# Kernel optimization log

Hardware: AMD Instinct MI355X
Metric: run time of the kernel (lower is better)

## Reference

```python
import jax, jax.numpy as jnp
import numpy as np

F8_MAX = 448.0  # max representable value of float8_e4m3fn


def setup_inputs() -> dict:
    key = jax.random.key(0)
    k1, k2, k3 = jax.random.split(key, 3)
    inp = jax.random.normal(k1, (4, 2048, 4096), dtype=jnp.float32)
    weight = jax.random.normal(k2, (4096, 16384), dtype=jnp.float32) * 0.02  # [in, out] (stored transposed)
    bias = jax.random.normal(k3, (16384,), dtype=jnp.float32)
    return {"inp": inp, "weight": weight, "bias": bias}


def reference(inp, weight, bias):
    # --- weight quantization (from_float with abs-max observer) ---
    w_scale = jnp.max(jnp.abs(weight)) / F8_MAX                      # scalar fp32
    w_q = (weight * (1.0 / w_scale)).astype(jnp.float8_e4m3fn)       # [in, out] fp8

    # --- dynamic input quantization: amax = max(|min|, |max|) ---
    x = inp.reshape(-1, inp.shape[-1])                               # [N, in]
    amax = jnp.maximum(jnp.abs(jnp.min(x)), jnp.abs(jnp.max(x)))
    x_scale = amax / F8_MAX
    x_q = (x * (1.0 / x_scale)).astype(jnp.float8_e4m3fn)            # [N, in] fp8

    # --- fp8_gemm_v2: dequant-matmul with fused scales + bias ---
    out = jnp.matmul(x_q.astype(jnp.float32), w_q.astype(jnp.float32))
    out = out * (x_scale * w_scale) + bias                           # [N, out]
    return out.reshape(inp.shape[:-1] + (weight.shape[1],))
```

## Files before the change

kernel.cpp:

```cpp
#include <hip/hip_runtime.h>
#include <stdint.h>
#include <stddef.h>

typedef float f32x16 __attribute__((ext_vector_type(16)));
typedef int i32x8 __attribute__((ext_vector_type(8)));

union Frag32 { long l[4]; i32x8 v; };


__global__ void absmax_kernel(const float4* __restrict__ x, size_t n4,
                              unsigned int* __restrict__ out) {
  size_t idx = ((size_t)blockIdx.x * blockDim.x + threadIdx.x) * 2;
  size_t stride = (size_t)gridDim.x * blockDim.x * 2;
  float m0 = 0.f, m1 = 0.f;
  for (size_t i = idx; i < n4; i += stride) {
    float4 v = x[i];
    float4 u = x[i + 1];
    m0 = fmaxf(m0, fmaxf(fmaxf(fabsf(v.x), fabsf(v.y)),
                         fmaxf(fabsf(v.z), fabsf(v.w))));
    m1 = fmaxf(m1, fmaxf(fmaxf(fabsf(u.x), fabsf(u.y)),
                         fmaxf(fabsf(u.z), fabsf(u.w))));
  }
  float m = fmaxf(m0, m1);
#pragma unroll
  for (int off = 32; off > 0; off >>= 1)
    m = fmaxf(m, __shfl_xor(m, off));
  if ((threadIdx.x & 63) == 0)
    atomicMax(out, __float_as_uint(m));
}

__global__ void quantize_x_kernel(const float4* __restrict__ x,
                                  uint8_t* __restrict__ xq,
                                  const unsigned int* __restrict__ amax,
                                  int K, int n_chunks) {
  const float x_scale = __uint_as_float(amax[1]) / 448.0f;
  const float inv = 1.0f / x_scale;
  const int kslots = K >> 5;
  int idx = blockIdx.x * blockDim.x + threadIdx.x;
  const int stride = gridDim.x * blockDim.x;
  for (; idx < n_chunks; idx += stride) {
    const int slot = idx >> 9;
    const int p16 = idx & 511;
    const int row = p16 >> 1;
    const int kkb0 = (p16 & 1) << 4;
    const int mblk = slot / kslots;
    const int ksl = slot - mblk * kslots;
    const size_t f4 = ((size_t)(mblk * 256 + row) * K + ksl * 32 + kkb0) >> 2;
    const float4 v0 = x[f4 + 0], v1 = x[f4 + 1], v2 = x[f4 + 2], v3 = x[f4 + 3];
    uint32_t c0 = __builtin_amdgcn_cvt_pk_fp8_f32(v0.x * inv, v0.y * inv, 0, false);
    c0 = __builtin_amdgcn_cvt_pk_fp8_f32(v0.z * inv, v0.w * inv, c0, true);
    uint32_t c1 = __builtin_amdgcn_cvt_pk_fp8_f32(v1.x * inv, v1.y * inv, 0, false);
    c1 = __builtin_amdgcn_cvt_pk_fp8_f32(v1.z * inv, v1.w * inv, c1, true);
    uint32_t c2 = __builtin_amdgcn_cvt_pk_fp8_f32(v2.x * inv, v2.y * inv, 0, false);
    c2 = __builtin_amdgcn_cvt_pk_fp8_f32(v2.z * inv, v2.w * inv, c2, true);
    uint32_t c3 = __builtin_amdgcn_cvt_pk_fp8_f32(v3.x * inv, v3.y * inv, 0, false);
    c3 = __builtin_amdgcn_cvt_pk_fp8_f32(v3.z * inv, v3.w * inv, c3, true);
    const int paddr = (row * 32 + kkb0) ^ (((row >> 2) & 1) << 4);
    uint4 o;
    o.x = c0; o.y = c1; o.z = c2; o.w = c3;
    *(uint4*)(xq + (size_t)slot * 8192 + paddr) = o;
  }
}

__global__ void quantize_wT_kernel(const float* __restrict__ w,
                                   uint8_t* __restrict__ wqt,
                                   const unsigned int* __restrict__ amax,
                                   int N, int K) {
  __shared__ float tileF[64][129];
  const float w_scale = __uint_as_float(amax[0]) / 448.0f;
  const float inv = 1.0f / w_scale;
  const int tn = blockIdx.x;
  const int tk = blockIdx.y;
  const int t = threadIdx.x;
  {
    const int nn4 = t & 15;
    const int kk0 = t >> 4;
#pragma unroll
    for (int i = 0; i < 8; ++i) {
      const int kk = kk0 + i * 16;
      const float4 v =
          *(const float4*)&w[(size_t)(tk * 128 + kk) * N + tn * 64 + nn4 * 4];
      tileF[nn4 * 4 + 0][kk] = v.x;
      tileF[nn4 * 4 + 1][kk] = v.y;
      tileF[nn4 * 4 + 2][kk] = v.z;
      tileF[nn4 * 4 + 3][kk] = v.w;
    }
  }
  __syncthreads();
  {
    const int n = t & 63;
    const int c = t >> 6;
    unsigned long long q[4];
#pragma unroll
    for (int cc = 0; cc < 4; ++cc) {
      const float4 u0 = *(const float4*)&tileF[n][c * 32 + cc * 8];
      const float4 u1 = *(const float4*)&tileF[n][c * 32 + cc * 8 + 4];
      uint32_t lo = __builtin_amdgcn_cvt_pk_fp8_f32(u0.x * inv, u0.y * inv, 0, false);
      lo = __builtin_amdgcn_cvt_pk_fp8_f32(u0.z * inv, u0.w * inv, lo, true);
      uint32_t hi = __builtin_amdgcn_cvt_pk_fp8_f32(u1.x * inv, u1.y * inv, 0, false);
      hi = __builtin_amdgcn_cvt_pk_fp8_f32(u1.z * inv, u1.w * inv, hi, true);
      q[cc] = (unsigned long long)lo | ((unsigned long long)hi << 32);
    }
    const int n_g = tn * 64 + n;
    const int k0g = tk * 128 + c * 32;
    const size_t slot = (size_t)(n_g >> 8) * (K >> 5) + (k0g >> 5);
    const int row = n_g & 255;
    const int bit = (row >> 2) & 1;
    uint8_t* pbase = wqt + slot * 8192 + row * 32;
    ulonglong2 s0, s1;
    s0.x = q[0]; s0.y = q[1];
    s1.x = q[2]; s1.y = q[3];
    *(ulonglong2*)(pbase + (bit << 4)) = s0;
    *(ulonglong2*)(pbase + ((bit ^ 1) << 4)) = s1;
  }
}

#define T_BM 256
#define T_BN 256
#define UNIT_SCALE 0x7F7F7F7F

__device__ __forceinline__ void gl_lds16(const uint8_t* g, uint8_t* lds) {
  __builtin_amdgcn_global_load_lds(
      (const __attribute__((address_space(1))) void*)g,
      (__attribute__((address_space(3))) void*)lds, 16, 0, 0);
}

__global__ __launch_bounds__(1024, 4) void gemm_fp8_mx(
    const uint8_t* __restrict__ Aq, const uint8_t* __restrict__ BqT,
    const float* __restrict__ bias, const unsigned int* __restrict__ amax,
    float* __restrict__ C, int M, int N, int K) {
  extern __shared__ uint8_t smem[];
  uint8_t* const Ar = smem;
  uint8_t* const Br = smem + 65536;

  const int ntn = N / T_BN;
  const int bid = blockIdx.x;
  const int m0 = (bid / ntn) * T_BM;
  const int n0 = (bid % ntn) * T_BN;

  const int tid = threadIdx.x;
  const int w = tid >> 6;
  const int l = tid & 63;
  const int wr = w >> 2;
  const int wc = w & 3;

  const int kslots = K >> 5;

  const int soff = w * 1024 + l * 16;
  const uint8_t* a_src = Aq + (size_t)(m0 >> 8) * kslots * 8192 + soff;
  const uint8_t* b_src = BqT + (size_t)(n0 >> 8) * kslots * 8192 + soff;

  const int h = l >> 5;
  const int rl = l & 31;
  int aoff[2][2], boff[2][2];
#pragma unroll
  for (int mt = 0; mt < 2; ++mt) {
    const int ra = wr * 64 + mt * 32 + rl;
    const int rb = wc * 64 + mt * 32 + rl;
#pragma unroll
    for (int c = 0; c < 2; ++c) {
      aoff[mt][c] = h * 8192 + ra * 32 + ((c ^ ((ra >> 2) & 1)) << 4);
      boff[mt][c] = h * 8192 + rb * 32 + ((c ^ ((rb >> 2) & 1)) << 4);
    }
  }

  f32x16 acc[2][2];
#pragma unroll
  for (int i = 0; i < 2; ++i)
#pragma unroll
    for (int j = 0; j < 2; ++j) acc[i][j] = 0.f;

  const int NP = K >> 6;

  gl_lds16(a_src, Ar + soff);
  gl_lds16(b_src, Br + soff);
  gl_lds16(a_src + 16384, Ar + 16384 + soff);
  gl_lds16(b_src + 16384, Br + 16384 + soff);
  asm volatile("s_waitcnt vmcnt(2)" ::: "memory");
  __builtin_amdgcn_s_barrier();

#define PHASE_(pp)                                                          \
  do {                                                                      \
    const int ss = ((pp) + 2 < NP) ? ((pp) + 2) : ((pp)-2);                 \
    const int rslot = (((pp) + 2) & 3) * 16384;                             \
    gl_lds16(a_src + (size_t)ss * 16384, Ar + rslot + soff);                \
    gl_lds16(b_src + (size_t)ss * 16384, Br + rslot + soff);                \
    const uint8_t* Asl = Ar + ((pp)&3) * 16384;                             \
    const uint8_t* Bsl = Br + ((pp)&3) * 16384;                             \
    Frag32 af[2], bf[2];                                                    \
    _Pragma("unroll") for (int mt = 0; mt < 2; ++mt) {                      \
      ulonglong2 ta0 = *(const ulonglong2*)(Asl + aoff[mt][0]);             \
      ulonglong2 ta1 = *(const ulonglong2*)(Asl + aoff[mt][1]);             \
      af[mt].l[0] = (long)ta0.x; af[mt].l[1] = (long)ta0.y;                 \
      af[mt].l[2] = (long)ta1.x; af[mt].l[3] = (long)ta1.y;                 \
      ulonglong2 tb0 = *(const ulonglong2*)(Bsl + boff[mt][0]);             \
      ulonglong2 tb1 = *(const ulonglong2*)(Bsl + boff[mt][1]);             \
      bf[mt].l[0] = (long)tb0.x; bf[mt].l[1] = (long)tb0.y;                 \
      bf[mt].l[2] = (long)tb1.x; bf[mt].l[3] = (long)tb1.y;                 \
    }                                                                       \
    __builtin_amdgcn_s_setprio(1);                                          \
    acc[0][0] = __builtin_amdgcn_mfma_scale_f32_32x32x64_f8f6f4(            \
        af[0].v, bf[0].v, acc[0][0], 0, 0, 0, UNIT_SCALE, 0, UNIT_SCALE);   \
    acc[1][0] = __builtin_amdgcn_mfma_scale_f32_32x32x64_f8f6f4(            \
        af[1].v, bf[0].v, acc[1][0], 0, 0, 0, UNIT_SCALE, 0, UNIT_SCALE);   \
    acc[0][1] = __builtin_amdgcn_mfma_scale_f32_32x32x64_f8f6f4(            \
        af[0].v, bf[1].v, acc[0][1], 0, 0, 0, UNIT_SCALE, 0, UNIT_SCALE);   \
    acc[1][1] = __builtin_amdgcn_mfma_scale_f32_32x32x64_f8f6f4(            \
        af[1].v, bf[1].v, acc[1][1], 0, 0, 0, UNIT_SCALE, 0, UNIT_SCALE);   \
    __builtin_amdgcn_s_setprio(0);                                          \
    asm volatile("s_waitcnt vmcnt(2)" ::: "memory");                        \
  } while (0)

  for (int p = 0; p < NP; p += 2) {
    PHASE_(p);
    PHASE_(p + 1);
    __builtin_amdgcn_s_barrier();
  }
  asm volatile("s_waitcnt vmcnt(0)" ::: "memory");

  const float x_scale = __uint_as_float(amax[1]) / 448.0f;
  const float w_scale = __uint_as_float(amax[0]) / 448.0f;
  const float s = x_scale * w_scale;
  const int colb = n0 + wc * 64 + rl;
  const int rowb = m0 + wr * 64 + 4 * h;
#pragma unroll
  for (int nt = 0; nt < 2; ++nt) {
    const int col = colb + nt * 32;
    const float bv = bias[col];
#pragma unroll
    for (int mt = 0; mt < 2; ++mt) {
#pragma unroll
      for (int r = 0; r < 16; ++r) {
        const int row = rowb + mt * 32 + (r & 3) + 8 * (r >> 2);
        C[(size_t)row * N + col] = acc[mt][nt][r] * s + bv;
      }
    }
  }
}

extern "C" void kernel_launch(void* const* d_in, const int* in_sizes, int n_in,
                              void* d_out, int out_size, void* d_ws, size_t ws_size,
                              hipStream_t stream) {
  const float* inp = (const float*)d_in[0];
  const float* weight = (const float*)d_in[1];
  const float* bias = (const float*)d_in[2];
  float* out = (float*)d_out;

  const int N = in_sizes[2];
  const int K = in_sizes[1] / N;
  const int M = in_sizes[0] / K;

  uint8_t* ws = (uint8_t*)d_ws;
  unsigned int* amax = (unsigned int*)ws;
  uint8_t* xq = ws + 256;
  uint8_t* wqt = ws + 256 + (size_t)M * K;

  hipMemsetAsync(d_ws, 0, 8, stream);

  absmax_kernel<<<2048, 256, 0, stream>>>((const float4*)weight,
                                          (size_t)K * N / 4, amax + 0);
  absmax_kernel<<<2048, 256, 0, stream>>>((const float4*)inp,
                                          (size_t)M * K / 4, amax + 1);

  quantize_x_kernel<<<4096, 256, 0, stream>>>((const float4*)inp, xq, amax,
                                              K, M * K / 16);
  quantize_wT_kernel<<<dim3(N / 64, K / 128), 256, 0, stream>>>(weight, wqt,
                                                                amax, N, K);

  gemm_fp8_mx<<<(M / T_BM) * (N / T_BN), 1024, 131072, stream>>>(
      xq, wqt, bias, amax, out, M, N, K);
}
```

Before: 904.9 us.

## Load B fragments straight from global, halve LDS, and remap workgroups across XCDs

The weight (B) operand tiles are no longer staged in LDS. Each wave reads its B fragments directly from global memory into registers, so shared memory drops to 64KB and holds only the A ring buffer. The pipeline becomes one phase per iteration with a barrier each step, and workgroup IDs are remapped so consecutive blocks on the same XCD share weight columns. The aim is to cut LDS traffic and footprint and to improve L2 locality. In exchange, each B fragment is fetched four times per workgroup from cache, and the global load latency is waited on in the same iteration that uses it.

```diff
diff --git a/kernel.cpp b/kernel.cpp
--- a/kernel.cpp
+++ b/kernel.cpp
@@ -131,12 +131,16 @@
     float* __restrict__ C, int M, int N, int K) {
   extern __shared__ uint8_t smem[];
   uint8_t* const Ar = smem;
-  uint8_t* const Br = smem + 65536;
-
-  const int ntn = N / T_BN;
+
+  const int nwg = gridDim.x;
+  const int cpx = nwg >> 3;
   const int bid = blockIdx.x;
-  const int m0 = (bid / ntn) * T_BM;
-  const int n0 = (bid % ntn) * T_BN;
+  const int wg = (bid & 7) * cpx + (bid >> 3);
+  const int ntm = M / T_BM;
+  const int tm = wg & (ntm - 1);
+  const int tn = wg / ntm;
+  const int m0 = tm * T_BM;
+  const int n0 = tn * T_BN;
 
   const int tid = threadIdx.x;
   const int w = tid >> 6;
@@ -148,7 +152,6 @@
 
   const int soff = w * 1024 + l * 16;
   const uint8_t* a_src = Aq + (size_t)(m0 >> 8) * kslots * 8192 + soff;
-  const uint8_t* b_src = BqT + (size_t)(n0 >> 8) * kslots * 8192 + soff;
 
   const int h = l >> 5;
   const int rl = l & 31;
@@ -163,6 +166,7 @@
       boff[mt][c] = h * 8192 + rb * 32 + ((c ^ ((rb >> 2) & 1)) << 4);
     }
   }
+  const uint8_t* b_blk = BqT + (size_t)(n0 >> 8) * kslots * 8192;
 
   f32x16 acc[2][2];
 #pragma unroll
@@ -173,47 +177,47 @@
   const int NP = K >> 6;
 
   gl_lds16(a_src, Ar + soff);
-  gl_lds16(b_src, Br + soff);
   gl_lds16(a_src + 16384, Ar + 16384 + soff);
-  gl_lds16(b_src + 16384, Br + 16384 + soff);
-  asm volatile("s_waitcnt vmcnt(2)" ::: "memory");
+  asm volatile("s_waitcnt vmcnt(1)" ::: "memory");
   __builtin_amdgcn_s_barrier();
 
-#define PHASE_(pp)                                                          \
-  do {                                                                      \
-    const int ss = ((pp) + 2 < NP) ? ((pp) + 2) : ((pp)-2);                 \
-    const int rslot = (((pp) + 2) & 3) * 16384;                             \
-    gl_lds16(a_src + (size_t)ss * 16384, Ar + rslot + soff);                \
-    gl_lds16(b_src + (size_t)ss * 16384, Br + rslot + soff);                \
-    const uint8_t* Asl = Ar + ((pp)&3) * 16384;                             \
-    const uint8_t* Bsl = Br + ((pp)&3) * 16384;                             \
-    Frag32 af[2], bf[2];                                                    \
-    _Pragma("unroll") for (int mt = 0; mt < 2; ++mt) {                      \
-      ulonglong2 ta0 = *(const ulonglong2*)(Asl + aoff[mt][0]);             \
-      ulonglong2 ta1 = *(const ulonglong2*)(Asl + aoff[mt][1]);             \
-      af[mt].l[0] = (long)ta0.x; af[mt].l[1] = (long)ta0.y;                 \
-      af[mt].l[2] = (long)ta1.x; af[mt].l[3] = (long)ta1.y;                 \
-      ulonglong2 tb0 = *(const ulonglong2*)(Bsl + boff[mt][0]);             \
-      ulonglong2 tb1 = *(const ulonglong2*)(Bsl + boff[mt][1]);             \
-      bf[mt].l[0] = (long)tb0.x; bf[mt].l[1] = (long)tb0.y;                 \
-      bf[mt].l[2] = (long)tb1.x; bf[mt].l[3] = (long)tb1.y;                 \
-    }                                                                       \
-    __builtin_amdgcn_s_setprio(1);                                          \
-    acc[0][0] = __builtin_amdgcn_mfma_scale_f32_32x32x64_f8f6f4(            \
-        af[0].v, bf[0].v, acc[0][0], 0, 0, 0, UNIT_SCALE, 0, UNIT_SCALE);   \
-    acc[1][0] = __builtin_amdgcn_mfma_scale_f32_32x32x64_f8f6f4(            \
-        af[1].v, bf[0].v, acc[1][0], 0, 0, 0, UNIT_SCALE, 0, UNIT_SCALE);   \
-    acc[0][1] = __builtin_amdgcn_mfma_scale_f32_32x32x64_f8f6f4(            \
-        af[0].v, bf[1].v, acc[0][1], 0, 0, 0, UNIT_SCALE, 0, UNIT_SCALE);   \
-    acc[1][1] = __builtin_amdgcn_mfma_scale_f32_32x32x64_f8f6f4(            \
-        af[1].v, bf[1].v, acc[1][1], 0, 0, 0, UNIT_SCALE, 0, UNIT_SCALE);   \
-    __builtin_amdgcn_s_setprio(0);                                          \
-    asm volatile("s_waitcnt vmcnt(2)" ::: "memory");                        \
-  } while (0)
-
-  for (int p = 0; p < NP; p += 2) {
-    PHASE_(p);
-    PHASE_(p + 1);
+  for (int p = 0; p < NP; ++p) {
+    const uint8_t* bp = b_blk + (size_t)p * 16384;
+    Frag32 bf[2];
+#pragma unroll
+    for (int mt = 0; mt < 2; ++mt) {
+      ulonglong2 t0 = *(const ulonglong2*)(bp + boff[mt][0]);
+      ulonglong2 t1 = *(const ulonglong2*)(bp + boff[mt][1]);
+      bf[mt].l[0] = (long)t0.x; bf[mt].l[1] = (long)t0.y;
+      bf[mt].l[2] = (long)t1.x; bf[mt].l[3] = (long)t1.y;
+    }
+
+    const int ss = (p + 2 < NP) ? (p + 2) : (NP - 1);
+    gl_lds16(a_src + (size_t)ss * 16384, Ar + ((p + 2) & 3) * 16384 + soff);
+
+    const uint8_t* Asl = Ar + (p & 3) * 16384;
+    Frag32 af[2];
+#pragma unroll
+    for (int mt = 0; mt < 2; ++mt) {
+      ulonglong2 t0 = *(const ulonglong2*)(Asl + aoff[mt][0]);
+      ulonglong2 t1 = *(const ulonglong2*)(Asl + aoff[mt][1]);
+      af[mt].l[0] = (long)t0.x; af[mt].l[1] = (long)t0.y;
+      af[mt].l[2] = (long)t1.x; af[mt].l[3] = (long)t1.y;
+    }
+
+    asm volatile("s_waitcnt vmcnt(1)" ::: "memory");
+
+    __builtin_amdgcn_s_setprio(1);
+    acc[0][0] = __builtin_amdgcn_mfma_scale_f32_32x32x64_f8f6f4(
+        af[0].v, bf[0].v, acc[0][0], 0, 0, 0, UNIT_SCALE, 0, UNIT_SCALE);
+    acc[1][0] = __builtin_amdgcn_mfma_scale_f32_32x32x64_f8f6f4(
+        af[1].v, bf[0].v, acc[1][0], 0, 0, 0, UNIT_SCALE, 0, UNIT_SCALE);
+    acc[0][1] = __builtin_amdgcn_mfma_scale_f32_32x32x64_f8f6f4(
+        af[0].v, bf[1].v, acc[0][1], 0, 0, 0, UNIT_SCALE, 0, UNIT_SCALE);
+    acc[1][1] = __builtin_amdgcn_mfma_scale_f32_32x32x64_f8f6f4(
+        af[1].v, bf[1].v, acc[1][1], 0, 0, 0, UNIT_SCALE, 0, UNIT_SCALE);
+    __builtin_amdgcn_s_setprio(0);
+
     __builtin_amdgcn_s_barrier();
   }
   asm volatile("s_waitcnt vmcnt(0)" ::: "memory");
@@ -267,6 +271,6 @@
   quantize_wT_kernel<<<dim3(N / 64, K / 128), 256, 0, stream>>>(weight, wqt,
                                                                 amax, N, K);
 
-  gemm_fp8_mx<<<(M / T_BM) * (N / T_BN), 1024, 131072, stream>>>(
+  gemm_fp8_mx<<<(M / T_BM) * (N / T_BN), 1024, 65536, stream>>>(
       xq, wqt, bias, amax, out, M, N, K);
 }
```

New measurement: 1.174 ms. 29.7% more time.
